# Performance work log

Measured on AMD Instinct MI355X. Metric: run time of the kernel, lower is better.

The kernel has to match this reference:

```python
import jax, jax.numpy as jnp
import numpy as np

N = 1_000_000
D_IN = 128
D_OUT = 128
S = 8192  # num_samples


def setup_inputs() -> dict:
    key = jax.random.key(0)
    k1, k2, k3, k4 = jax.random.split(key, 4)
    element_embeddings = jax.random.normal(k1, (N, D_IN), dtype=jnp.float32)
    w_att = jax.random.normal(k2, (D_IN,), dtype=jnp.float32) * (1.0 / np.sqrt(D_IN))
    w_out = jax.random.normal(k3, (D_OUT, D_IN), dtype=jnp.float32) * (1.0 / np.sqrt(D_IN))
    element_to_sample_map = jax.random.randint(k4, (N,), 0, S, dtype=jnp.int32)
    return {
        "element_embeddings": element_embeddings,
        "w_att": w_att,
        "w_out": w_out,
        "element_to_sample_map": element_to_sample_map,
        "num_samples": S,
    }


def reference(element_embeddings, w_att, w_out, element_to_sample_map, num_samples):
    idx = element_to_sample_map
    # attention scores: Linear(D_in, 1, bias=False) -> [N]
    scores = element_embeddings @ w_att  # [N]
    # scatter log-softmax over segments (eps=0), numerically stable
    seg_max = jax.ops.segment_max(scores, idx, num_segments=num_samples)  # [S]
    shifted = scores - seg_max[idx]  # [N]
    seg_sumexp = jax.ops.segment_sum(jnp.exp(shifted), idx, num_segments=num_samples)  # [S]
    attention_probs = jnp.exp(shifted - jnp.log(seg_sumexp)[idx])  # [N]
    # output projection then weighted scatter-sum pooling
    projected = element_embeddings @ w_out.T  # [N, D_out]
    return jax.ops.segment_sum(projected * attention_probs[:, None], idx, num_segments=num_samples)  # [S, D_out]
```

## Files before the change

kernel.cpp:

```cpp
#include <hip/hip_runtime.h>
#include <math.h>

#define CAP 256

__global__ __launch_bounds__(256) void k_scatterB(const int* __restrict__ idx,
                                                  int* __restrict__ cursor,
                                                  int* __restrict__ bucket, int n) {
    int i = blockIdx.x * 256 + threadIdx.x;
    if (i < n) {
        int s = idx[i];
        int pos = atomicAdd(&cursor[s], 1);
        if (pos < CAP) bucket[(size_t)s * CAP + pos] = i;
    }
}

__global__ __launch_bounds__(256, 4) void k_pool(
        const float* __restrict__ emb, const float* __restrict__ w_att,
        const int* __restrict__ cursor, const int* __restrict__ bucket,
        float* __restrict__ pooled, int S) {
    int wave = (blockIdx.x << 2) | (threadIdx.x >> 6);
    int lane = threadIdx.x & 63;
    if (wave >= S) return;
    int g   = lane >> 4;
    int l16 = lane & 15;
    int cnt = min(cursor[wave], CAP);
    const int* ob = bucket + (size_t)wave * CAP;
    const float* wrow = w_att + 8 * l16;
    float4 wa0 = *reinterpret_cast<const float4*>(wrow);
    float4 wa1 = *reinterpret_cast<const float4*>(wrow + 4);
    float4 a0 = make_float4(0.f, 0.f, 0.f, 0.f);
    float4 a1 = make_float4(0.f, 0.f, 0.f, 0.f);
    float Z = 0.f;
    if (cnt > 0) {
        int last = cnt - 1;
        int e = g;
        int i0 = ob[min(e, last)];
        const float* r = emb + (size_t)i0 * 128 + 8 * l16;
        float4 v0 = *reinterpret_cast<const float4*>(r);
        float4 v1 = *reinterpret_cast<const float4*>(r + 4);
        int nit = (cnt + 3) >> 2;
        for (int it = 0; it < nit; ++it) {
            int en = e + 4;
            int inext = ob[min(en, last)];
            const float* rn = emb + (size_t)inext * 128 + 8 * l16;
            float4 n0 = *reinterpret_cast<const float4*>(rn);
            float4 n1 = *reinterpret_cast<const float4*>(rn + 4);
            float part = v0.x * wa0.x + v0.y * wa0.y + v0.z * wa0.z + v0.w * wa0.w
                       + v1.x * wa1.x + v1.y * wa1.y + v1.z * wa1.z + v1.w * wa1.w;
            part += __shfl_xor(part, 1);
            part += __shfl_xor(part, 2);
            part += __shfl_xor(part, 4);
            part += __shfl_xor(part, 8);
            float ex = (e <= last) ? __expf(part) : 0.f;
            Z += ex;
            a0.x = fmaf(ex, v0.x, a0.x);
            a0.y = fmaf(ex, v0.y, a0.y);
            a0.z = fmaf(ex, v0.z, a0.z);
            a0.w = fmaf(ex, v0.w, a0.w);
            a1.x = fmaf(ex, v1.x, a1.x);
            a1.y = fmaf(ex, v1.y, a1.y);
            a1.z = fmaf(ex, v1.z, a1.z);
            a1.w = fmaf(ex, v1.w, a1.w);
            v0 = n0;
            v1 = n1;
            e = en;
        }
    }
#pragma unroll
    for (int m = 16; m <= 32; m <<= 1) {
        a0.x += __shfl_xor(a0.x, m);
        a0.y += __shfl_xor(a0.y, m);
        a0.z += __shfl_xor(a0.z, m);
        a0.w += __shfl_xor(a0.w, m);
        a1.x += __shfl_xor(a1.x, m);
        a1.y += __shfl_xor(a1.y, m);
        a1.z += __shfl_xor(a1.z, m);
        a1.w += __shfl_xor(a1.w, m);
        Z    += __shfl_xor(Z,    m);
    }
    float rn_ = (Z > 0.f) ? (1.0f / Z) : 0.f;
    if (g == 0) {
        float* o = pooled + (size_t)wave * 128 + 8 * l16;
        *reinterpret_cast<float4*>(o)     = make_float4(a0.x * rn_, a0.y * rn_, a0.z * rn_, a0.w * rn_);
        *reinterpret_cast<float4*>(o + 4) = make_float4(a1.x * rn_, a1.y * rn_, a1.z * rn_, a1.w * rn_);
    }
}

#define SPB 8
__global__ __launch_bounds__(256, 4) void k_proj(
        const float* __restrict__ w_out, float* __restrict__ io, int S) {
    __shared__ float wl[128][68];
    __shared__ float pl[SPB][64];
    int t = threadIdx.x;
    int d = t & 127;
    int h = t >> 7;
    int s0 = blockIdx.x * SPB;
    float acc[4] = {0.f, 0.f, 0.f, 0.f};

    for (int ph = 0; ph < 2; ++ph) {
        __syncthreads();
        for (int j = t; j < 2048; j += 256) {
            int r = j >> 4, c4 = j & 15;
            float4 wv = reinterpret_cast<const float4*>(w_out + (size_t)r * 128 + ph * 64)[c4];
            *reinterpret_cast<float4*>(&wl[r][c4 * 4]) = wv;
        }
        if (t < 128) {
            int sm = t >> 4, c4 = t & 15;
            int ss = s0 + sm;
            float4 pv = (ss < S)
                ? reinterpret_cast<const float4*>(io + (size_t)ss * 128 + ph * 64)[c4]
                : make_float4(0.f, 0.f, 0.f, 0.f);
            *reinterpret_cast<float4*>(&pl[sm][c4 * 4]) = pv;
        }
        __syncthreads();
#pragma unroll
        for (int k4 = 0; k4 < 16; ++k4) {
            float4 wv = *reinterpret_cast<const float4*>(&wl[d][k4 * 4]);
#pragma unroll
            for (int j = 0; j < 4; ++j) {
                float4 pv = *reinterpret_cast<const float4*>(&pl[2 * j + h][k4 * 4]);
                acc[j] = fmaf(wv.x, pv.x, acc[j]);
                acc[j] = fmaf(wv.y, pv.y, acc[j]);
                acc[j] = fmaf(wv.z, pv.z, acc[j]);
                acc[j] = fmaf(wv.w, pv.w, acc[j]);
            }
        }
    }
#pragma unroll
    for (int j = 0; j < 4; ++j) {
        int s = s0 + 2 * j + h;
        if (s < S) io[(size_t)s * 128 + d] = acc[j];
    }
}

extern "C" void kernel_launch(void* const* d_in, const int* in_sizes, int n_in,
                              void* d_out, int out_size, void* d_ws, size_t ws_size,
                              hipStream_t stream) {
    const float* emb   = (const float*)d_in[0];
    const float* w_att = (const float*)d_in[1];
    const float* w_out = (const float*)d_in[2];
    const int*   idx   = (const int*)d_in[3];
    const int N = in_sizes[0] / 128;
    const int S = out_size / 128;

    char* ws = (char*)d_ws;
    int* cursor = (int*)(ws + 0);
    int* bucket = (int*)(ws + 64 * 1024);
    float* out  = (float*)d_out;

    hipMemsetAsync(cursor, 0, (size_t)S * sizeof(int), stream);
    k_scatterB<<<(N + 255) / 256, 256, 0, stream>>>(idx, cursor, bucket, N);
    k_pool    <<<(S + 3) / 4, 256, 0, stream>>>(emb, w_att, cursor, bucket, out, S);
    k_proj    <<<(S + SPB - 1) / SPB, 256, 0, stream>>>(w_out, out, S);
}
```

Baseline: 299.3 us.

## Fuse bucketing, pooling and projection into one cooperative persistent kernel

Replaces the memset plus three kernel launches with a single cooperative kernel of 1024 blocks that zeroes cursors, scatters element indices into buckets, pools each sample, and applies the output projection, with grid-wide syncs between phases. It also changes the lane-to-column mapping so each lane loads two float4s 64 floats apart instead of eight contiguous floats. The aim is to remove launch gaps and memset overhead. In exchange it adds grid barriers, fixes parallelism at 1024 persistent blocks, and keeps the original multi-kernel path as a fallback if the cooperative launch fails.

```diff
diff --git a/kernel.cpp b/kernel.cpp
--- a/kernel.cpp
+++ b/kernel.cpp
@@ -1,7 +1,157 @@
 #include <hip/hip_runtime.h>
+#include <hip/hip_cooperative_groups.h>
 #include <math.h>
 
-#define CAP 256
+namespace cg = cooperative_groups;
+
+#define CAP   256
+#define NBLK  1024
+#define TPB   256
+#define SPB   8
+
+
+__device__ __forceinline__ void pool_one_sample(
+        int sW, int g, int l16, const float* __restrict__ emb,
+        const float4& wa0, const float4& wa1,
+        const int* __restrict__ cursor, const int* __restrict__ bucket,
+        float* __restrict__ out) {
+    int cnt = min(cursor[sW], CAP);
+    const int* ob = bucket + (size_t)sW * CAP;
+    float4 a0 = make_float4(0.f, 0.f, 0.f, 0.f);
+    float4 a1 = make_float4(0.f, 0.f, 0.f, 0.f);
+    float Z = 0.f;
+    if (cnt > 0) {
+        int last = cnt - 1;
+        int e = g;
+        int i0 = ob[min(e, last)];
+        const float* r = emb + (size_t)i0 * 128;
+        float4 v0 = *reinterpret_cast<const float4*>(r + 4 * l16);
+        float4 v1 = *reinterpret_cast<const float4*>(r + 64 + 4 * l16);
+        int nit = (cnt + 3) >> 2;
+        for (int it = 0; it < nit; ++it) {
+            int en = e + 4;
+            int inx = ob[min(en, last)];
+            const float* rn = emb + (size_t)inx * 128;
+            float4 n0 = *reinterpret_cast<const float4*>(rn + 4 * l16);
+            float4 n1 = *reinterpret_cast<const float4*>(rn + 64 + 4 * l16);
+            float part = v0.x * wa0.x + v0.y * wa0.y + v0.z * wa0.z + v0.w * wa0.w
+                       + v1.x * wa1.x + v1.y * wa1.y + v1.z * wa1.z + v1.w * wa1.w;
+            part += __shfl_xor(part, 1);
+            part += __shfl_xor(part, 2);
+            part += __shfl_xor(part, 4);
+            part += __shfl_xor(part, 8);
+            float ex = (e <= last) ? __expf(part) : 0.f;
+            Z += ex;
+            a0.x = fmaf(ex, v0.x, a0.x); a0.y = fmaf(ex, v0.y, a0.y);
+            a0.z = fmaf(ex, v0.z, a0.z); a0.w = fmaf(ex, v0.w, a0.w);
+            a1.x = fmaf(ex, v1.x, a1.x); a1.y = fmaf(ex, v1.y, a1.y);
+            a1.z = fmaf(ex, v1.z, a1.z); a1.w = fmaf(ex, v1.w, a1.w);
+            v0 = n0; v1 = n1; e = en;
+        }
+    }
+#pragma unroll
+    for (int m = 16; m <= 32; m <<= 1) {
+        a0.x += __shfl_xor(a0.x, m); a0.y += __shfl_xor(a0.y, m);
+        a0.z += __shfl_xor(a0.z, m); a0.w += __shfl_xor(a0.w, m);
+        a1.x += __shfl_xor(a1.x, m); a1.y += __shfl_xor(a1.y, m);
+        a1.z += __shfl_xor(a1.z, m); a1.w += __shfl_xor(a1.w, m);
+        Z    += __shfl_xor(Z, m);
+    }
+    float rn_ = (Z > 0.f) ? (1.0f / Z) : 0.f;
+    if (g == 0) {
+        float* o = out + (size_t)sW * 128;
+        *reinterpret_cast<float4*>(o + 4 * l16) =
+            make_float4(a0.x * rn_, a0.y * rn_, a0.z * rn_, a0.w * rn_);
+        *reinterpret_cast<float4*>(o + 64 + 4 * l16) =
+            make_float4(a1.x * rn_, a1.y * rn_, a1.z * rn_, a1.w * rn_);
+    }
+}
+
+__device__ __forceinline__ void proj_block(
+        int s0, int t, const float* __restrict__ w_out,
+        float* __restrict__ io, int S,
+        float (*wl)[68], float (*pl)[64]) {
+    int d = t & 127;
+    int h = t >> 7;
+    float acc[4] = {0.f, 0.f, 0.f, 0.f};
+    for (int ph = 0; ph < 2; ++ph) {
+        __syncthreads();
+        for (int j = t; j < 2048; j += TPB) {
+            int r = j >> 4, c4 = j & 15;
+            float4 wv = reinterpret_cast<const float4*>(w_out + (size_t)r * 128 + ph * 64)[c4];
+            *reinterpret_cast<float4*>(&wl[r][c4 * 4]) = wv;
+        }
+        if (t < 128) {
+            int sm = t >> 4, c4 = t & 15;
+            int ss = s0 + sm;
+            float4 pv = (ss < S)
+                ? reinterpret_cast<const float4*>(io + (size_t)ss * 128 + ph * 64)[c4]
+                : make_float4(0.f, 0.f, 0.f, 0.f);
+            *reinterpret_cast<float4*>(&pl[sm][c4 * 4]) = pv;
+        }
+        __syncthreads();
+#pragma unroll
+        for (int k4 = 0; k4 < 16; ++k4) {
+            float4 wv = *reinterpret_cast<const float4*>(&wl[d][k4 * 4]);
+#pragma unroll
+            for (int j = 0; j < 4; ++j) {
+                float4 pv = *reinterpret_cast<const float4*>(&pl[2 * j + h][k4 * 4]);
+                acc[j] = fmaf(wv.x, pv.x, acc[j]);
+                acc[j] = fmaf(wv.y, pv.y, acc[j]);
+                acc[j] = fmaf(wv.z, pv.z, acc[j]);
+                acc[j] = fmaf(wv.w, pv.w, acc[j]);
+            }
+        }
+    }
+#pragma unroll
+    for (int j = 0; j < 4; ++j) {
+        int s = s0 + 2 * j + h;
+        if (s < S) io[(size_t)s * 128 + d] = acc[j];
+    }
+}
+
+__global__ __launch_bounds__(TPB, 4) void k_fused(
+        const float* __restrict__ emb, const float* __restrict__ w_att,
+        const float* __restrict__ w_out, const int* __restrict__ idx,
+        int* __restrict__ cursor, int* __restrict__ bucket,
+        float* __restrict__ out, int N, int S) {
+    __shared__ float wl[128][68];
+    __shared__ float pl[SPB][64];
+    cg::grid_group grid = cg::this_grid();
+    const int t = threadIdx.x;
+    const int b = blockIdx.x;
+    const int gtid = b * TPB + t;
+    const int NT = NBLK * TPB;
+
+    for (int s = gtid; s < S; s += NT) cursor[s] = 0;
+    grid.sync();
+
+    for (int i = gtid; i < N; i += NT) {
+        int s = idx[i];
+        int pos = atomicAdd(&cursor[s], 1);
+        if (pos < CAP) bucket[(size_t)s * CAP + pos] = i;
+    }
+    grid.sync();
+
+    {
+        int wave = (b << 2) | (t >> 6);
+        int lane = t & 63;
+        int g = lane >> 4, l16 = lane & 15;
+        float4 wa0 = *reinterpret_cast<const float4*>(w_att + 4 * l16);
+        float4 wa1 = *reinterpret_cast<const float4*>(w_att + 64 + 4 * l16);
+        for (int sW = wave; sW < S; sW += NBLK * 4)
+            pool_one_sample(sW, g, l16, emb, wa0, wa1, cursor, bucket, out);
+    }
+    grid.sync();
+
+    for (int s0 = b * SPB; s0 < S; s0 += NBLK * SPB)
+        proj_block(s0, t, w_out, out, S, wl, pl);
+}
+
+__global__ __launch_bounds__(256) void k_zero(int* __restrict__ cursor, int S) {
+    int i = blockIdx.x * 256 + threadIdx.x;
+    if (i < S) cursor[i] = 0;
+}
 
 __global__ __launch_bounds__(256) void k_scatterB(const int* __restrict__ idx,
                                                   int* __restrict__ cursor,
@@ -14,123 +164,24 @@
     }
 }
 
-__global__ __launch_bounds__(256, 4) void k_pool(
+__global__ __launch_bounds__(256, 4) void k_poolF(
         const float* __restrict__ emb, const float* __restrict__ w_att,
         const int* __restrict__ cursor, const int* __restrict__ bucket,
-        float* __restrict__ pooled, int S) {
+        float* __restrict__ out, int S) {
     int wave = (blockIdx.x << 2) | (threadIdx.x >> 6);
     int lane = threadIdx.x & 63;
     if (wave >= S) return;
-    int g   = lane >> 4;
-    int l16 = lane & 15;
-    int cnt = min(cursor[wave], CAP);
-    const int* ob = bucket + (size_t)wave * CAP;
-    const float* wrow = w_att + 8 * l16;
-    float4 wa0 = *reinterpret_cast<const float4*>(wrow);
-    float4 wa1 = *reinterpret_cast<const float4*>(wrow + 4);
-    float4 a0 = make_float4(0.f, 0.f, 0.f, 0.f);
-    float4 a1 = make_float4(0.f, 0.f, 0.f, 0.f);
-    float Z = 0.f;
-    if (cnt > 0) {
-        int last = cnt - 1;
-        int e = g;
-        int i0 = ob[min(e, last)];
-        const float* r = emb + (size_t)i0 * 128 + 8 * l16;
-        float4 v0 = *reinterpret_cast<const float4*>(r);
-        float4 v1 = *reinterpret_cast<const float4*>(r + 4);
-        int nit = (cnt + 3) >> 2;
-        for (int it = 0; it < nit; ++it) {
-            int en = e + 4;
-            int inext = ob[min(en, last)];
-            const float* rn = emb + (size_t)inext * 128 + 8 * l16;
-            float4 n0 = *reinterpret_cast<const float4*>(rn);
-            float4 n1 = *reinterpret_cast<const float4*>(rn + 4);
-            float part = v0.x * wa0.x + v0.y * wa0.y + v0.z * wa0.z + v0.w * wa0.w
-                       + v1.x * wa1.x + v1.y * wa1.y + v1.z * wa1.z + v1.w * wa1.w;
-            part += __shfl_xor(part, 1);
-            part += __shfl_xor(part, 2);
-            part += __shfl_xor(part, 4);
-            part += __shfl_xor(part, 8);
-            float ex = (e <= last) ? __expf(part) : 0.f;
-            Z += ex;
-            a0.x = fmaf(ex, v0.x, a0.x);
-            a0.y = fmaf(ex, v0.y, a0.y);
-            a0.z = fmaf(ex, v0.z, a0.z);
-            a0.w = fmaf(ex, v0.w, a0.w);
-            a1.x = fmaf(ex, v1.x, a1.x);
-            a1.y = fmaf(ex, v1.y, a1.y);
-            a1.z = fmaf(ex, v1.z, a1.z);
-            a1.w = fmaf(ex, v1.w, a1.w);
-            v0 = n0;
-            v1 = n1;
-            e = en;
-        }
-    }
-#pragma unroll
-    for (int m = 16; m <= 32; m <<= 1) {
-        a0.x += __shfl_xor(a0.x, m);
-        a0.y += __shfl_xor(a0.y, m);
-        a0.z += __shfl_xor(a0.z, m);
-        a0.w += __shfl_xor(a0.w, m);
-        a1.x += __shfl_xor(a1.x, m);
-        a1.y += __shfl_xor(a1.y, m);
-        a1.z += __shfl_xor(a1.z, m);
-        a1.w += __shfl_xor(a1.w, m);
-        Z    += __shfl_xor(Z,    m);
-    }
-    float rn_ = (Z > 0.f) ? (1.0f / Z) : 0.f;
-    if (g == 0) {
-        float* o = pooled + (size_t)wave * 128 + 8 * l16;
-        *reinterpret_cast<float4*>(o)     = make_float4(a0.x * rn_, a0.y * rn_, a0.z * rn_, a0.w * rn_);
-        *reinterpret_cast<float4*>(o + 4) = make_float4(a1.x * rn_, a1.y * rn_, a1.z * rn_, a1.w * rn_);
-    }
-}
-
-#define SPB 8
-__global__ __launch_bounds__(256, 4) void k_proj(
+    int g = lane >> 4, l16 = lane & 15;
+    float4 wa0 = *reinterpret_cast<const float4*>(w_att + 4 * l16);
+    float4 wa1 = *reinterpret_cast<const float4*>(w_att + 64 + 4 * l16);
+    pool_one_sample(wave, g, l16, emb, wa0, wa1, cursor, bucket, out);
+}
+
+__global__ __launch_bounds__(256, 4) void k_projF(
         const float* __restrict__ w_out, float* __restrict__ io, int S) {
     __shared__ float wl[128][68];
     __shared__ float pl[SPB][64];
-    int t = threadIdx.x;
-    int d = t & 127;
-    int h = t >> 7;
-    int s0 = blockIdx.x * SPB;
-    float acc[4] = {0.f, 0.f, 0.f, 0.f};
-
-    for (int ph = 0; ph < 2; ++ph) {
-        __syncthreads();
-        for (int j = t; j < 2048; j += 256) {
-            int r = j >> 4, c4 = j & 15;
-            float4 wv = reinterpret_cast<const float4*>(w_out + (size_t)r * 128 + ph * 64)[c4];
-            *reinterpret_cast<float4*>(&wl[r][c4 * 4]) = wv;
-        }
-        if (t < 128) {
-            int sm = t >> 4, c4 = t & 15;
-            int ss = s0 + sm;
-            float4 pv = (ss < S)
-                ? reinterpret_cast<const float4*>(io + (size_t)ss * 128 + ph * 64)[c4]
-                : make_float4(0.f, 0.f, 0.f, 0.f);
-            *reinterpret_cast<float4*>(&pl[sm][c4 * 4]) = pv;
-        }
-        __syncthreads();
-#pragma unroll
-        for (int k4 = 0; k4 < 16; ++k4) {
-            float4 wv = *reinterpret_cast<const float4*>(&wl[d][k4 * 4]);
-#pragma unroll
-            for (int j = 0; j < 4; ++j) {
-                float4 pv = *reinterpret_cast<const float4*>(&pl[2 * j + h][k4 * 4]);
-                acc[j] = fmaf(wv.x, pv.x, acc[j]);
-                acc[j] = fmaf(wv.y, pv.y, acc[j]);
-                acc[j] = fmaf(wv.z, pv.z, acc[j]);
-                acc[j] = fmaf(wv.w, pv.w, acc[j]);
-            }
-        }
-    }
-#pragma unroll
-    for (int j = 0; j < 4; ++j) {
-        int s = s0 + 2 * j + h;
-        if (s < S) io[(size_t)s * 128 + d] = acc[j];
-    }
+    proj_block(blockIdx.x * SPB, threadIdx.x, w_out, io, S, wl, pl);
 }
 
 extern "C" void kernel_launch(void* const* d_in, const int* in_sizes, int n_in,
@@ -140,16 +191,24 @@
     const float* w_att = (const float*)d_in[1];
     const float* w_out = (const float*)d_in[2];
     const int*   idx   = (const int*)d_in[3];
-    const int N = in_sizes[0] / 128;
-    const int S = out_size / 128;
+    int N = in_sizes[0] / 128;
+    int S = out_size / 128;
 
     char* ws = (char*)d_ws;
     int* cursor = (int*)(ws + 0);
     int* bucket = (int*)(ws + 64 * 1024);
     float* out  = (float*)d_out;
 
-    hipMemsetAsync(cursor, 0, (size_t)S * sizeof(int), stream);
-    k_scatterB<<<(N + 255) / 256, 256, 0, stream>>>(idx, cursor, bucket, N);
-    k_pool    <<<(S + 3) / 4, 256, 0, stream>>>(emb, w_att, cursor, bucket, out, S);
-    k_proj    <<<(S + SPB - 1) / SPB, 256, 0, stream>>>(w_out, out, S);
-}
+    void* args[] = {(void*)&emb, (void*)&w_att, (void*)&w_out, (void*)&idx,
+                    (void*)&cursor, (void*)&bucket, (void*)&out,
+                    (void*)&N, (void*)&S};
+    hipError_t err = hipLaunchCooperativeKernel((const void*)k_fused,
+                                                dim3(NBLK), dim3(TPB),
+                                                args, 0, stream);
+    if (err != hipSuccess) {
+        k_zero    <<<(S + 255) / 256, 256, 0, stream>>>(cursor, S);
+        k_scatterB<<<(N + 255) / 256, 256, 0, stream>>>(idx, cursor, bucket, N);
+        k_poolF   <<<(S + 3) / 4, 256, 0, stream>>>(emb, w_att, cursor, bucket, out, S);
+        k_projF   <<<(S + SPB - 1) / SPB, 256, 0, stream>>>(w_out, out, S);
+    }
+}
```

After: 473.9 us. +58.3%, slower.

## Preload bucket indices into registers and deepen gather prefetch in pooling kernel

Applied to the files above, without the earlier changes.

The pooling kernel now loads all 256 bucket indices up front, four per lane, and hands them out with shuffles, so the loop no longer issues a dependent global index load each step. It prefetches embedding rows two iterations ahead instead of one, giving the gather loads more time in flight. Each lane now reads two float4s split across the two halves of the row instead of eight contiguous floats, which changes the coalescing pattern. Occupancy is raised to 8 waves per SIMD. The added registers for the indices and the extra prefetch stage may push register usage against the new launch bound.

```diff
diff --git a/kernel.cpp b/kernel.cpp
--- a/kernel.cpp
+++ b/kernel.cpp
@@ -2,6 +2,7 @@
 #include <math.h>
 
 #define CAP 256
+#define SPB 8
 
 __global__ __launch_bounds__(256) void k_scatterB(const int* __restrict__ idx,
                                                   int* __restrict__ cursor,
@@ -14,7 +15,7 @@
     }
 }
 
-__global__ __launch_bounds__(256, 4) void k_pool(
+__global__ __launch_bounds__(256, 8) void k_pool(
         const float* __restrict__ emb, const float* __restrict__ w_att,
         const int* __restrict__ cursor, const int* __restrict__ bucket,
         float* __restrict__ pooled, int S) {
@@ -25,68 +26,84 @@
     int l16 = lane & 15;
     int cnt = min(cursor[wave], CAP);
     const int* ob = bucket + (size_t)wave * CAP;
-    const float* wrow = w_att + 8 * l16;
-    float4 wa0 = *reinterpret_cast<const float4*>(wrow);
-    float4 wa1 = *reinterpret_cast<const float4*>(wrow + 4);
+    int i0 = ob[lane];
+    int i1 = ob[lane + 64];
+    int i2 = ob[lane + 128];
+    int i3 = ob[lane + 192];
+    float4 wa0 = *reinterpret_cast<const float4*>(w_att + 4 * l16);
+    float4 wa1 = *reinterpret_cast<const float4*>(w_att + 64 + 4 * l16);
     float4 a0 = make_float4(0.f, 0.f, 0.f, 0.f);
     float4 a1 = make_float4(0.f, 0.f, 0.f, 0.f);
     float Z = 0.f;
     if (cnt > 0) {
         int last = cnt - 1;
-        int e = g;
-        int i0 = ob[min(e, last)];
-        const float* r = emb + (size_t)i0 * 128 + 8 * l16;
-        float4 v0 = *reinterpret_cast<const float4*>(r);
-        float4 v1 = *reinterpret_cast<const float4*>(r + 4);
-        int nit = (cnt + 3) >> 2;
-        for (int it = 0; it < nit; ++it) {
-            int en = e + 4;
-            int inext = ob[min(en, last)];
-            const float* rn = emb + (size_t)inext * 128 + 8 * l16;
-            float4 n0 = *reinterpret_cast<const float4*>(rn);
-            float4 n1 = *reinterpret_cast<const float4*>(rn + 4);
+        int nit  = (cnt + 3) >> 2;
+        auto fetch_idx = [&](int t) -> int {
+            int p    = min(4 * t + g, last);
+            int src  = p & 63;
+            int slot = p >> 6;
+            int r0 = __shfl(i0, src);
+            int r1 = __shfl(i1, src);
+            int r2 = __shfl(i2, src);
+            int r3 = __shfl(i3, src);
+            int lo = (slot & 1) ? r1 : r0;
+            int hi = (slot & 1) ? r3 : r2;
+            return (slot & 2) ? hi : lo;
+        };
+        int e0 = fetch_idx(0);
+        const float* r0p = emb + (size_t)e0 * 128;
+        float4 v0 = *reinterpret_cast<const float4*>(r0p + 4 * l16);
+        float4 v1 = *reinterpret_cast<const float4*>(r0p + 64 + 4 * l16);
+        float4 u0 = v0, u1 = v1;
+        if (nit > 1) {
+            int e1 = fetch_idx(1);
+            const float* r1p = emb + (size_t)e1 * 128;
+            u0 = *reinterpret_cast<const float4*>(r1p + 4 * l16);
+            u1 = *reinterpret_cast<const float4*>(r1p + 64 + 4 * l16);
+        }
+        for (int t = 0; t < nit; ++t) {
+            float4 n0 = u0, n1 = u1;
+            if (t + 2 < nit) {
+                int e2 = fetch_idx(t + 2);
+                const float* rn = emb + (size_t)e2 * 128;
+                n0 = *reinterpret_cast<const float4*>(rn + 4 * l16);
+                n1 = *reinterpret_cast<const float4*>(rn + 64 + 4 * l16);
+            }
+            int p = 4 * t + g;
             float part = v0.x * wa0.x + v0.y * wa0.y + v0.z * wa0.z + v0.w * wa0.w
                        + v1.x * wa1.x + v1.y * wa1.y + v1.z * wa1.z + v1.w * wa1.w;
             part += __shfl_xor(part, 1);
             part += __shfl_xor(part, 2);
             part += __shfl_xor(part, 4);
             part += __shfl_xor(part, 8);
-            float ex = (e <= last) ? __expf(part) : 0.f;
+            float ex = (p <= last) ? __expf(part) : 0.f;
             Z += ex;
-            a0.x = fmaf(ex, v0.x, a0.x);
-            a0.y = fmaf(ex, v0.y, a0.y);
-            a0.z = fmaf(ex, v0.z, a0.z);
-            a0.w = fmaf(ex, v0.w, a0.w);
-            a1.x = fmaf(ex, v1.x, a1.x);
-            a1.y = fmaf(ex, v1.y, a1.y);
-            a1.z = fmaf(ex, v1.z, a1.z);
-            a1.w = fmaf(ex, v1.w, a1.w);
-            v0 = n0;
-            v1 = n1;
-            e = en;
+            a0.x = fmaf(ex, v0.x, a0.x); a0.y = fmaf(ex, v0.y, a0.y);
+            a0.z = fmaf(ex, v0.z, a0.z); a0.w = fmaf(ex, v0.w, a0.w);
+            a1.x = fmaf(ex, v1.x, a1.x); a1.y = fmaf(ex, v1.y, a1.y);
+            a1.z = fmaf(ex, v1.z, a1.z); a1.w = fmaf(ex, v1.w, a1.w);
+            v0 = u0; v1 = u1;
+            u0 = n0; u1 = n1;
         }
     }
 #pragma unroll
     for (int m = 16; m <= 32; m <<= 1) {
-        a0.x += __shfl_xor(a0.x, m);
-        a0.y += __shfl_xor(a0.y, m);
-        a0.z += __shfl_xor(a0.z, m);
-        a0.w += __shfl_xor(a0.w, m);
-        a1.x += __shfl_xor(a1.x, m);
-        a1.y += __shfl_xor(a1.y, m);
-        a1.z += __shfl_xor(a1.z, m);
-        a1.w += __shfl_xor(a1.w, m);
-        Z    += __shfl_xor(Z,    m);
+        a0.x += __shfl_xor(a0.x, m); a0.y += __shfl_xor(a0.y, m);
+        a0.z += __shfl_xor(a0.z, m); a0.w += __shfl_xor(a0.w, m);
+        a1.x += __shfl_xor(a1.x, m); a1.y += __shfl_xor(a1.y, m);
+        a1.z += __shfl_xor(a1.z, m); a1.w += __shfl_xor(a1.w, m);
+        Z    += __shfl_xor(Z, m);
     }
     float rn_ = (Z > 0.f) ? (1.0f / Z) : 0.f;
     if (g == 0) {
-        float* o = pooled + (size_t)wave * 128 + 8 * l16;
-        *reinterpret_cast<float4*>(o)     = make_float4(a0.x * rn_, a0.y * rn_, a0.z * rn_, a0.w * rn_);
-        *reinterpret_cast<float4*>(o + 4) = make_float4(a1.x * rn_, a1.y * rn_, a1.z * rn_, a1.w * rn_);
+        float* o = pooled + (size_t)wave * 128;
+        *reinterpret_cast<float4*>(o + 4 * l16) =
+            make_float4(a0.x * rn_, a0.y * rn_, a0.z * rn_, a0.w * rn_);
+        *reinterpret_cast<float4*>(o + 64 + 4 * l16) =
+            make_float4(a1.x * rn_, a1.y * rn_, a1.z * rn_, a1.w * rn_);
     }
 }
 
-#define SPB 8
 __global__ __launch_bounds__(256, 4) void k_proj(
         const float* __restrict__ w_out, float* __restrict__ io, int S) {
     __shared__ float wl[128][68];
```

Result: no change. 296.3 us (-1.0%).
